# Kernel tuning notes

Measured on AMD Instinct MI355X. Metric: run time of the kernel, lower is better.

## Reference

```python
import jax, jax.numpy as jnp
import numpy as np

N_NODES = 50000
N_EDGES = 800000
D = 64


def setup_inputs() -> dict:
    key = jax.random.key(0)
    ks = jax.random.split(key, 8)
    x = jax.random.normal(ks[0], (N_NODES, D), dtype=jnp.float32)
    src = jax.random.randint(ks[1], (N_EDGES,), 0, N_NODES, dtype=jnp.int32)
    dst = jax.random.randint(ks[2], (N_EDGES,), 0, N_NODES, dtype=jnp.int32)
    s = 1.0 / np.sqrt(D)
    w1_0 = jax.random.uniform(ks[3], (D, D), jnp.float32, -s, s)
    w2_0 = jax.random.uniform(ks[4], (D, D), jnp.float32, -s, s)
    w1_1 = jax.random.uniform(ks[5], (D, D), jnp.float32, -s, s)
    w2_1 = jax.random.uniform(ks[6], (D, D), jnp.float32, -s, s)
    b = jnp.zeros((D,), jnp.float32)
    return {"x": x, "src": src, "dst": dst,
            "w1_0": w1_0, "b1_0": b, "w2_0": w2_0, "b2_0": b,
            "w1_1": w1_1, "b1_1": b, "w2_1": w2_1, "b2_1": b}


def _gin_layer(x, src, dst, w1, b1, w2, b2):
    # sum aggregation over edges: agg[i] = sum_{(j->i) in E} x[j]
    agg = jax.ops.segment_sum(x[src], dst, num_segments=N_NODES)
    h = x + agg  # (1 + eps) * x + agg, eps = 0 (DGL GINConv default)
    h = jnp.tanh(h @ w1 + b1)
    return h @ w2 + b2


def reference(x, src, dst, w1_0, b1_0, w2_0, b2_0, w1_1, b1_1, w2_1, b2_1):
    x = _gin_layer(x, src, dst, w1_0, b1_0, w2_0, b2_0)
    x = _gin_layer(x, src, dst, w1_1, b1_1, w2_1, b2_1)
    return x
```

## Files before the change

### kernel.cpp

```cpp
#include <hip/hip_runtime.h>

#define D 64
#define CAP 56

typedef __attribute__((ext_vector_type(8))) short short8;
typedef __attribute__((ext_vector_type(4))) float f32x4;

__device__ __forceinline__ unsigned short f2bf(float f) {
    unsigned u = __float_as_uint(f);
    u = (u + 0x7fff + ((u >> 16) & 1)) >> 16;
    return (unsigned short)u;
}
__device__ __forceinline__ float bf_lo(unsigned u) { return __uint_as_float(u << 16); }
__device__ __forceinline__ float bf_hi(unsigned u) { return __uint_as_float(u & 0xffff0000u); }

__global__ __launch_bounds__(256) void prep_scatter_kernel(
    const int* __restrict__ src, const int* __restrict__ dst,
    int* __restrict__ deg, unsigned short* __restrict__ buf, int n_edges, int nsb,
    const float* __restrict__ x, unsigned short* __restrict__ xb, int n4, int ncb,
    const float* __restrict__ w1_0, const float* __restrict__ w2_0,
    const float* __restrict__ w1_1, const float* __restrict__ w2_1,
    unsigned short* __restrict__ wt)
{
    const int b = blockIdx.x;
    if (b < nsb) {
        int e = b * 256 + threadIdx.x;
        if (e < n_edges) {
            int d = dst[e];
            int p = atomicAdd(&deg[d], 1);
            if (p < CAP) buf[(size_t)d * CAP + p] = (unsigned short)src[e];
        }
    } else if (b < nsb + ncb) {
        int i = (b - nsb) * 256 + threadIdx.x;
        if (i < n4) {
            float4 v = *(const float4*)(x + i * 4);
            ushort4 o;
            o.x = f2bf(v.x); o.y = f2bf(v.y); o.z = f2bf(v.z); o.w = f2bf(v.w);
            *(ushort4*)(xb + i * 4) = o;
        }
    } else {
        int i = (b - nsb - ncb) * 256 + threadIdx.x;
        int m = i >> 12, r = i & 4095;
        int n = r >> 6, k = r & 63;
        const float* w = (m == 0) ? w1_0 : (m == 1) ? w2_0 : (m == 2) ? w1_1 : w2_1;
        wt[i] = f2bf(w[k * 64 + n]);
    }
}

__global__ __launch_bounds__(256) void gather_kernel(
    const unsigned short* __restrict__ xb, const int* __restrict__ deg,
    const unsigned short* __restrict__ buf, unsigned short* __restrict__ aggb)
{
    const int tid  = threadIdx.x;
    const int lane = tid & 63;
    const int wave = tid >> 6;
    const int n    = blockIdx.x * 4 + wave;

    const int slot = lane >> 3;
    const int fc   = (lane & 7) << 3;

    int my_idx = buf[(size_t)n * CAP + (lane < CAP ? lane : CAP - 1)];
    int dd = deg[n];
    dd = dd < CAP ? dd : CAP;

    uint4 u = make_uint4(0u, 0u, 0u, 0u);
    if (slot == 0) u = *(const uint4*)(xb + (size_t)n * D + fc);

    int s[7];
    #pragma unroll
    for (int g = 0; g < 7; ++g) s[g] = __shfl(my_idx, (g << 3) + slot);

    uint4 v[7];
    #pragma unroll
    for (int g = 0; g < 7; ++g)
        v[g] = *(const uint4*)(xb + (size_t)s[g] * D + fc);

    float a[8] = {0.f, 0.f, 0.f, 0.f, 0.f, 0.f, 0.f, 0.f};
    #pragma unroll
    for (int g = 0; g < 7; ++g) {
        float m = ((g << 3) + slot) < dd ? 1.0f : 0.0f;
        a[0] += bf_lo(v[g].x) * m; a[1] += bf_hi(v[g].x) * m;
        a[2] += bf_lo(v[g].y) * m; a[3] += bf_hi(v[g].y) * m;
        a[4] += bf_lo(v[g].z) * m; a[5] += bf_hi(v[g].z) * m;
        a[6] += bf_lo(v[g].w) * m; a[7] += bf_hi(v[g].w) * m;
    }
    a[0] += bf_lo(u.x); a[1] += bf_hi(u.x);
    a[2] += bf_lo(u.y); a[3] += bf_hi(u.y);
    a[4] += bf_lo(u.z); a[5] += bf_hi(u.z);
    a[6] += bf_lo(u.w); a[7] += bf_hi(u.w);

    #pragma unroll
    for (int m = 8; m <= 32; m <<= 1) {
        #pragma unroll
        for (int q = 0; q < 8; ++q) a[q] += __shfl_xor(a[q], m);
    }
    if (slot == 0) {
        uint4 o;
        o.x = (unsigned)f2bf(a[0]) | ((unsigned)f2bf(a[1]) << 16);
        o.y = (unsigned)f2bf(a[2]) | ((unsigned)f2bf(a[3]) << 16);
        o.z = (unsigned)f2bf(a[4]) | ((unsigned)f2bf(a[5]) << 16);
        o.w = (unsigned)f2bf(a[6]) | ((unsigned)f2bf(a[7]) << 16);
        *(uint4*)(aggb + (size_t)n * D + fc) = o;
    }
}

template <bool WRITE_BF16>
__global__ __launch_bounds__(256) void gin_dense_mfma(
    const unsigned short* __restrict__ hb, int n_nodes,
    const unsigned short* __restrict__ w1t, const float* __restrict__ b1,
    const unsigned short* __restrict__ w2t, const float* __restrict__ b2,
    float* __restrict__ out_f, unsigned short* __restrict__ out_b)
{
    __shared__ unsigned short sh [64][72];
    __shared__ unsigned short st [64][72];
    __shared__ unsigned short sw1[64][72];
    __shared__ unsigned short sw2[64][72];

    const int t    = threadIdx.x;
    const int lane = t & 63;
    const int wave = t >> 6;
    const int quad = lane >> 4;
    const int col  = lane & 15;
    const int nb   = blockIdx.x * 64;

    for (int c = t; c < 512; c += 256) {
        int row = c >> 3, c8 = (c & 7) << 3;
        *(uint4*)&sh [row][c8] = *(const uint4*)(hb  + (size_t)(nb + row) * D + c8);
        *(uint4*)&sw1[row][c8] = *(const uint4*)(w1t + row * D + c8);
        *(uint4*)&sw2[row][c8] = *(const uint4*)(w2t + row * D + c8);
    }
    __syncthreads();

    const int arow = 16 * wave + col;
    const int koff = quad << 3;

    short8 a0 = *(const short8*)&sh[arow][koff];
    short8 a1 = *(const short8*)&sh[arow][32 + koff];

    #pragma unroll
    for (int nt = 0; nt < 4; ++nt) {
        int n = (nt << 4) + col;
        short8 bw0 = *(const short8*)&sw1[n][koff];
        short8 bw1 = *(const short8*)&sw1[n][32 + koff];
        float bv = b1[n];
        f32x4 c = {bv, bv, bv, bv};
        c = __builtin_amdgcn_mfma_f32_16x16x32_bf16(a0, bw0, c, 0, 0, 0);
        c = __builtin_amdgcn_mfma_f32_16x16x32_bf16(a1, bw1, c, 0, 0, 0);
        #pragma unroll
        for (int r = 0; r < 4; ++r)
            st[16 * wave + (quad << 2) + r][n] = f2bf(tanhf(c[r]));
    }

    short8 p0 = *(const short8*)&st[arow][koff];
    short8 p1 = *(const short8*)&st[arow][32 + koff];

    #pragma unroll
    for (int nt = 0; nt < 4; ++nt) {
        int n = (nt << 4) + col;
        short8 bw0 = *(const short8*)&sw2[n][koff];
        short8 bw1 = *(const short8*)&sw2[n][32 + koff];
        float bv = b2[n];
        f32x4 c = {bv, bv, bv, bv};
        c = __builtin_amdgcn_mfma_f32_16x16x32_bf16(p0, bw0, c, 0, 0, 0);
        c = __builtin_amdgcn_mfma_f32_16x16x32_bf16(p1, bw1, c, 0, 0, 0);
        #pragma unroll
        for (int r = 0; r < 4; ++r) {
            int row = nb + 16 * wave + (quad << 2) + r;
            if (WRITE_BF16) {
                out_b[(size_t)row * D + n] = f2bf(c[r]);
            } else if (row < n_nodes) {
                out_f[(size_t)row * D + n] = c[r];
            }
        }
    }
}

extern "C" void kernel_launch(void* const* d_in, const int* in_sizes, int n_in,
                              void* d_out, int out_size, void* d_ws, size_t ws_size,
                              hipStream_t stream)
{
    const float* x    = (const float*)d_in[0];
    const int*   src  = (const int*)  d_in[1];
    const int*   dst  = (const int*)  d_in[2];
    const float* w1_0 = (const float*)d_in[3];
    const float* b1_0 = (const float*)d_in[4];
    const float* w2_0 = (const float*)d_in[5];
    const float* b2_0 = (const float*)d_in[6];
    const float* w1_1 = (const float*)d_in[7];
    const float* b1_1 = (const float*)d_in[8];
    const float* w2_1 = (const float*)d_in[9];
    const float* b2_1 = (const float*)d_in[10];
    float* out = (float*)d_out;

    const int n_nodes = in_sizes[0] / D;
    const int n_edges = in_sizes[1];
    const int n_pad   = (n_nodes + 63) & ~63;

    int*            deg  = (int*)d_ws;
    unsigned short* buf  = (unsigned short*)(deg + n_nodes);
    unsigned short* aggb = buf  + (size_t)n_nodes * CAP;
    unsigned short* xb   = aggb + (size_t)n_pad * D;
    unsigned short* x1b  = xb   + (size_t)n_pad * D;
    unsigned short* wt   = x1b  + (size_t)n_pad * D;

    const int n4  = n_nodes * D / 4;
    const int nsb = (n_edges + 255) / 256;
    const int ncb = (n4 + 255) / 256;

    hipMemsetAsync(deg, 0, (size_t)n_nodes * sizeof(int) + (size_t)n_nodes * CAP * sizeof(unsigned short), stream);
    prep_scatter_kernel<<<nsb + ncb + 64, 256, 0, stream>>>(
        src, dst, deg, buf, n_edges, nsb,
        x, xb, n4, ncb,
        w1_0, w2_0, w1_1, w2_1, wt);

    const int gather_blocks = n_nodes / 4;
    const int dense_blocks  = n_pad / 64;

    gather_kernel<<<gather_blocks, 256, 0, stream>>>(xb, deg, buf, aggb);
    gin_dense_mfma<true><<<dense_blocks, 256, 0, stream>>>(
        aggb, n_nodes, wt, b1_0, wt + 4096, b2_0, nullptr, x1b);
    gather_kernel<<<gather_blocks, 256, 0, stream>>>(x1b, deg, buf, aggb);
    gin_dense_mfma<false><<<dense_blocks, 256, 0, stream>>>(
        aggb, n_nodes, wt + 8192, b1_1, wt + 12288, b2_1, out, nullptr);
}
```

Before: 189.9 us.

## Fuse neighbor gather into dense MFMA kernel, removing separate gather pass

The standalone gather kernel is removed, and each 64-node dense block now performs its own neighbor aggregation. The block stages each node's neighbor index list and degree in LDS. Groups of 8 lanes then loop over the real degree, four neighbor rows at a time, and write the sum back into the shared tile before the two MFMA matmuls. This removes two kernel launches and the aggb global write and read per layer, and skips masked padding loads. In exchange there are far fewer, LDS-heavier blocks and a serial per-node loop, so less memory-level parallelism is available to hide gather latency.

```diff
diff --git a/kernel.cpp b/kernel.cpp
--- a/kernel.cpp
+++ b/kernel.cpp
@@ -47,66 +47,10 @@
     }
 }
 
-__global__ __launch_bounds__(256) void gather_kernel(
-    const unsigned short* __restrict__ xb, const int* __restrict__ deg,
-    const unsigned short* __restrict__ buf, unsigned short* __restrict__ aggb)
-{
-    const int tid  = threadIdx.x;
-    const int lane = tid & 63;
-    const int wave = tid >> 6;
-    const int n    = blockIdx.x * 4 + wave;
-
-    const int slot = lane >> 3;
-    const int fc   = (lane & 7) << 3;
-
-    int my_idx = buf[(size_t)n * CAP + (lane < CAP ? lane : CAP - 1)];
-    int dd = deg[n];
-    dd = dd < CAP ? dd : CAP;
-
-    uint4 u = make_uint4(0u, 0u, 0u, 0u);
-    if (slot == 0) u = *(const uint4*)(xb + (size_t)n * D + fc);
-
-    int s[7];
-    #pragma unroll
-    for (int g = 0; g < 7; ++g) s[g] = __shfl(my_idx, (g << 3) + slot);
-
-    uint4 v[7];
-    #pragma unroll
-    for (int g = 0; g < 7; ++g)
-        v[g] = *(const uint4*)(xb + (size_t)s[g] * D + fc);
-
-    float a[8] = {0.f, 0.f, 0.f, 0.f, 0.f, 0.f, 0.f, 0.f};
-    #pragma unroll
-    for (int g = 0; g < 7; ++g) {
-        float m = ((g << 3) + slot) < dd ? 1.0f : 0.0f;
-        a[0] += bf_lo(v[g].x) * m; a[1] += bf_hi(v[g].x) * m;
-        a[2] += bf_lo(v[g].y) * m; a[3] += bf_hi(v[g].y) * m;
-        a[4] += bf_lo(v[g].z) * m; a[5] += bf_hi(v[g].z) * m;
-        a[6] += bf_lo(v[g].w) * m; a[7] += bf_hi(v[g].w) * m;
-    }
-    a[0] += bf_lo(u.x); a[1] += bf_hi(u.x);
-    a[2] += bf_lo(u.y); a[3] += bf_hi(u.y);
-    a[4] += bf_lo(u.z); a[5] += bf_hi(u.z);
-    a[6] += bf_lo(u.w); a[7] += bf_hi(u.w);
-
-    #pragma unroll
-    for (int m = 8; m <= 32; m <<= 1) {
-        #pragma unroll
-        for (int q = 0; q < 8; ++q) a[q] += __shfl_xor(a[q], m);
-    }
-    if (slot == 0) {
-        uint4 o;
-        o.x = (unsigned)f2bf(a[0]) | ((unsigned)f2bf(a[1]) << 16);
-        o.y = (unsigned)f2bf(a[2]) | ((unsigned)f2bf(a[3]) << 16);
-        o.z = (unsigned)f2bf(a[4]) | ((unsigned)f2bf(a[5]) << 16);
-        o.w = (unsigned)f2bf(a[6]) | ((unsigned)f2bf(a[7]) << 16);
-        *(uint4*)(aggb + (size_t)n * D + fc) = o;
-    }
-}
-
 template <bool WRITE_BF16>
-__global__ __launch_bounds__(256) void gin_dense_mfma(
+__global__ __launch_bounds__(256) void gin_fused_mfma(
     const unsigned short* __restrict__ hb, int n_nodes,
+    const int* __restrict__ deg, const unsigned short* __restrict__ buf,
     const unsigned short* __restrict__ w1t, const float* __restrict__ b1,
     const unsigned short* __restrict__ w2t, const float* __restrict__ b2,
     float* __restrict__ out_f, unsigned short* __restrict__ out_b)
@@ -115,22 +59,78 @@
     __shared__ unsigned short st [64][72];
     __shared__ unsigned short sw1[64][72];
     __shared__ unsigned short sw2[64][72];
+    __shared__ __align__(16) unsigned short sidx[64][56];
+    __shared__ int sdeg[64];
 
     const int t    = threadIdx.x;
     const int lane = t & 63;
     const int wave = t >> 6;
+    const int nb   = blockIdx.x * 64;
+
+    {
+        const uint4* gsrc = (const uint4*)(buf + (size_t)nb * CAP);
+        uint4* ldst = (uint4*)&sidx[0][0];
+        for (int i = t; i < 448; i += 256) ldst[i] = gsrc[i];
+    }
+    if (t < 64) {
+        int gn = nb + t;
+        int dd = (gn < n_nodes) ? deg[gn] : 0;
+        sdeg[t] = dd < CAP ? dd : CAP;
+    }
+    for (int c = t; c < 512; c += 256) {
+        int row = c >> 3, c8 = (c & 7) << 3;
+        int gn = nb + row; if (gn >= n_nodes) gn = n_nodes - 1;
+        *(uint4*)&sh [row][c8] = *(const uint4*)(hb  + (size_t)gn * D + c8);
+        *(uint4*)&sw1[row][c8] = *(const uint4*)(w1t + row * D + c8);
+        *(uint4*)&sw2[row][c8] = *(const uint4*)(w2t + row * D + c8);
+    }
+    __syncthreads();
+
+    const int q  = lane >> 3;
+    const int fc = (lane & 7) << 3;
+
+    #pragma unroll
+    for (int p = 0; p < 2; ++p) {
+        const int m = 16 * wave + (p << 3) + q;
+        uint4 u = *(const uint4*)&sh[m][fc];
+        float a0 = bf_lo(u.x), a1 = bf_hi(u.x), a2 = bf_lo(u.y), a3 = bf_hi(u.y);
+        float a4 = bf_lo(u.z), a5 = bf_hi(u.z), a6 = bf_lo(u.w), a7 = bf_hi(u.w);
+        const int dd = sdeg[m];
+        const unsigned short* ip = sidx[m];
+        int j = 0;
+        for (; j + 4 <= dd; j += 4) {
+            int s0 = ip[j], s1 = ip[j + 1], s2 = ip[j + 2], s3 = ip[j + 3];
+            uint4 v0 = *(const uint4*)(hb + (size_t)s0 * D + fc);
+            uint4 v1 = *(const uint4*)(hb + (size_t)s1 * D + fc);
+            uint4 v2 = *(const uint4*)(hb + (size_t)s2 * D + fc);
+            uint4 v3 = *(const uint4*)(hb + (size_t)s3 * D + fc);
+            a0 += bf_lo(v0.x) + bf_lo(v1.x) + bf_lo(v2.x) + bf_lo(v3.x);
+            a1 += bf_hi(v0.x) + bf_hi(v1.x) + bf_hi(v2.x) + bf_hi(v3.x);
+            a2 += bf_lo(v0.y) + bf_lo(v1.y) + bf_lo(v2.y) + bf_lo(v3.y);
+            a3 += bf_hi(v0.y) + bf_hi(v1.y) + bf_hi(v2.y) + bf_hi(v3.y);
+            a4 += bf_lo(v0.z) + bf_lo(v1.z) + bf_lo(v2.z) + bf_lo(v3.z);
+            a5 += bf_hi(v0.z) + bf_hi(v1.z) + bf_hi(v2.z) + bf_hi(v3.z);
+            a6 += bf_lo(v0.w) + bf_lo(v1.w) + bf_lo(v2.w) + bf_lo(v3.w);
+            a7 += bf_hi(v0.w) + bf_hi(v1.w) + bf_hi(v2.w) + bf_hi(v3.w);
+        }
+        for (; j < dd; ++j) {
+            int s = ip[j];
+            uint4 v = *(const uint4*)(hb + (size_t)s * D + fc);
+            a0 += bf_lo(v.x); a1 += bf_hi(v.x);
+            a2 += bf_lo(v.y); a3 += bf_hi(v.y);
+            a4 += bf_lo(v.z); a5 += bf_hi(v.z);
+            a6 += bf_lo(v.w); a7 += bf_hi(v.w);
+        }
+        uint4 o;
+        o.x = (unsigned)f2bf(a0) | ((unsigned)f2bf(a1) << 16);
+        o.y = (unsigned)f2bf(a2) | ((unsigned)f2bf(a3) << 16);
+        o.z = (unsigned)f2bf(a4) | ((unsigned)f2bf(a5) << 16);
+        o.w = (unsigned)f2bf(a6) | ((unsigned)f2bf(a7) << 16);
+        *(uint4*)&sh[m][fc] = o;
+    }
+
     const int quad = lane >> 4;
     const int col  = lane & 15;
-    const int nb   = blockIdx.x * 64;
-
-    for (int c = t; c < 512; c += 256) {
-        int row = c >> 3, c8 = (c & 7) << 3;
-        *(uint4*)&sh [row][c8] = *(const uint4*)(hb  + (size_t)(nb + row) * D + c8);
-        *(uint4*)&sw1[row][c8] = *(const uint4*)(w1t + row * D + c8);
-        *(uint4*)&sw2[row][c8] = *(const uint4*)(w2t + row * D + c8);
-    }
-    __syncthreads();
-
     const int arow = 16 * wave + col;
     const int koff = quad << 3;
 
@@ -196,12 +196,11 @@
     const int n_edges = in_sizes[1];
     const int n_pad   = (n_nodes + 63) & ~63;
 
-    int*            deg  = (int*)d_ws;
-    unsigned short* buf  = (unsigned short*)(deg + n_nodes);
-    unsigned short* aggb = buf  + (size_t)n_nodes * CAP;
-    unsigned short* xb   = aggb + (size_t)n_pad * D;
-    unsigned short* x1b  = xb   + (size_t)n_pad * D;
-    unsigned short* wt   = x1b  + (size_t)n_pad * D;
+    int*            deg = (int*)d_ws;
+    unsigned short* buf = (unsigned short*)(deg + n_nodes);
+    unsigned short* xb  = buf + (size_t)n_nodes * CAP;
+    unsigned short* x1b = xb  + (size_t)n_pad * D;
+    unsigned short* wt  = x1b + (size_t)n_pad * D;
 
     const int n4  = n_nodes * D / 4;
     const int nsb = (n_edges + 255) / 256;
@@ -213,13 +212,10 @@
         x, xb, n4, ncb,
         w1_0, w2_0, w1_1, w2_1, wt);
 
-    const int gather_blocks = n_nodes / 4;
-    const int dense_blocks  = n_pad / 64;
-
-    gather_kernel<<<gather_blocks, 256, 0, stream>>>(xb, deg, buf, aggb);
-    gin_dense_mfma<true><<<dense_blocks, 256, 0, stream>>>(
-        aggb, n_nodes, wt, b1_0, wt + 4096, b2_0, nullptr, x1b);
-    gather_kernel<<<gather_blocks, 256, 0, stream>>>(x1b, deg, buf, aggb);
-    gin_dense_mfma<false><<<dense_blocks, 256, 0, stream>>>(
-        aggb, n_nodes, wt + 8192, b1_1, wt + 12288, b2_1, out, nullptr);
-}
+    const int fused_blocks = n_pad / 64;
+
+    gin_fused_mfma<true><<<fused_blocks, 256, 0, stream>>>(
+        xb, n_nodes, deg, buf, wt, b1_0, wt + 4096, b2_0, nullptr, x1b);
+    gin_fused_mfma<false><<<fused_blocks, 256, 0, stream>>>(
+        x1b, n_nodes, deg, buf, wt + 8192, b1_1, wt + 12288, b2_1, out, nullptr);
+}
```

Measured after the change: 189.6 us. Within noise of the previous version (-0.2%).
